# Kernel optimization log

Hardware: AMD Instinct MI355X
Metric: run time of the kernel (lower is better)

Reference implementation:

```python
import jax, jax.numpy as jnp
import numpy as np

D = 1024

def setup_inputs() -> dict:
    key = jax.random.key(0)
    ks = jax.random.split(key, 9)
    s = 1.0 / np.sqrt(D)
    return {
        "x": jax.random.normal(ks[0], (4, 2048, D), dtype=jnp.float32),
        "y": jax.random.normal(ks[1], (4, 2048, D), dtype=jnp.float32),
        "z": jax.random.normal(ks[2], (4, 2048, D), dtype=jnp.float32),
        "Wq": jax.random.uniform(ks[3], (D, D), jnp.float32, -s, s),
        "bq": jax.random.uniform(ks[4], (D,), jnp.float32, -s, s),
        "Wk": jax.random.uniform(ks[5], (D, D), jnp.float32, -s, s),
        "bk": jax.random.uniform(ks[6], (D,), jnp.float32, -s, s),
        "Wv": jax.random.uniform(ks[7], (D, D), jnp.float32, -s, s),
        "bv": jax.random.uniform(ks[8], (D,), jnp.float32, -s, s),
    }

def reference(x, y, z, Wq, bq, Wk, bk, Wv, bv):
    # nn.Linear: x @ W^T + b
    Q = jnp.einsum('bsd,ed->bse', x, Wq) + bq  # [B,S,D]
    K = jnp.einsum('bsd,ed->bse', y, Wk) + bk
    V = jnp.einsum('bsd,ed->bse', z, Wv) + bv
    scores = jnp.einsum('bqd,bkd->bqk', Q, K) / jnp.sqrt(jnp.float32(Q.shape[-1]))
    weights = jax.nn.softmax(scores, axis=-1)  # [B,S,S]
    return jnp.einsum('bqk,bkd->bqd', weights, V)
```

## Files before the change

kernel.cpp:

```cpp
#include <hip/hip_runtime.h>
#include <hip/hip_bf16.h>

typedef unsigned short u16;
typedef __bf16 bf16x8 __attribute__((ext_vector_type(8)));
typedef float  f32x4  __attribute__((ext_vector_type(4)));
typedef u16    u16x8  __attribute__((ext_vector_type(8)));

__device__ __forceinline__ u16 f2bf(float f) {
    unsigned u = __float_as_uint(f);
    u = (u + 0x7fffu + ((u >> 16) & 1u)) >> 16;
    return (u16)u;
}
__device__ __forceinline__ float bf2f(u16 h) {
    return __uint_as_float(((unsigned)h) << 16);
}

__global__ __launch_bounds__(256) void cvt3_bf16_kernel(
    const float* __restrict__ s0, const float* __restrict__ s1,
    const float* __restrict__ s2, u16* __restrict__ dst, size_t dstride, int n8)
{
    int i = blockIdx.x * 256 + threadIdx.x;
    if (i >= n8) return;
    const float* src = (blockIdx.z == 0) ? s0 : (blockIdx.z == 1) ? s1 : s2;
    u16* d = dst + (size_t)blockIdx.z * dstride;
    const float4* s4 = (const float4*)src;
    float4 a = s4[2 * i], b = s4[2 * i + 1];
    u16x8 o;
    o[0] = f2bf(a.x); o[1] = f2bf(a.y); o[2] = f2bf(a.z); o[3] = f2bf(a.w);
    o[4] = f2bf(b.x); o[5] = f2bf(b.y); o[6] = f2bf(b.z); o[7] = f2bf(b.w);
    ((u16x8*)d)[i] = o;
}

#define BUF_U 12288
#define LDS_B (3 * BUF_U * 2)

__device__ __forceinline__ void gload_lds16(const void* g, void* l) {
    __builtin_amdgcn_global_load_lds(
        (__attribute__((address_space(1))) void*)g,
        (__attribute__((address_space(3))) void*)l, 16, 0, 0);
}

__device__ __forceinline__ int swz_g(int r) {
    return (r & 3) ^ (((r >> 2) & 1) << 1) ^ ((r >> 3) & 1);
}

template<bool OUT_BF16, bool HAS_BIAS>
__global__ __launch_bounds__(512, 4) void gemm_k32(
    const u16* __restrict__ A, const u16* __restrict__ Bm,
    const float* __restrict__ bias, void* __restrict__ C,
    int M, int N, int K, float scale,
    long long aBS, long long bBS, long long cBS)
{
    extern __shared__ u16 lds[];

    const int gx = gridDim.x, gy = gridDim.y;
    const int slab = gx * gy;
    const int nwg  = slab * gridDim.z;
    const int b    = blockIdx.x + gx * (blockIdx.y + gy * blockIdx.z);
    const int qc   = nwg >> 3;
    const int L    = (b & 7) * qc + (b >> 3);
    const int tz   = L / slab;
    const int rr   = L - tz * slab;
    const int g4   = rr / (gx * 4);
    const int w4   = rr - g4 * (gx * 4);
    const int tx   = w4 >> 2;
    const int ty   = g4 * 4 + (w4 & 3);

    A  += (size_t)tz * aBS;
    Bm += (size_t)tz * bBS;

    const int m0 = ty * 256;
    const int n0 = tx * 128;
    const int tid  = threadIdx.x;
    const int lane = tid & 63;
    const int wave = tid >> 6;
    const int wm   = wave >> 1;
    const int wn   = wave & 1;
    const int fr   = lane & 15;
    const int kg   = lane >> 4;

    const int r_ = tid >> 2;
    const int s_ = (tid & 3) ^ swz_g(r_);
    const u16* gA = A  + (size_t)(m0 + r_) * K + s_ * 8;
    const u16* gB = Bm + (size_t)(n0 + r_) * K + s_ * 8;
    const int dstW = wave * 512;

    auto stA = [&](u16* bufb, int tk, int c) {
        gload_lds16(gA + (size_t)c * 128 * K + tk * 32, bufb + c * 4096 + dstW);
    };
    auto stB = [&](u16* bufb, int tk) {
        gload_lds16(gB + tk * 32, bufb + 8192 + dstW);
    };

    auto rdA = [&](const u16* sa, int m) {
        const int R  = wm * 64 + m * 16 + fr;
        const int sl = kg ^ swz_g(R);
        return *(const bf16x8*)&sa[R * 32 + sl * 8];
    };
    auto rdB = [&](const u16* sb, int n) {
        const int R  = wn * 64 + n * 16 + fr;
        const int sl = kg ^ swz_g(R);
        return *(const bf16x8*)&sb[R * 32 + sl * 8];
    };

    f32x4 acc[4][4] = {};
    const int NT = K / 32;

    u16 *p0 = lds, *p1 = lds + BUF_U, *p2 = lds + 2 * BUF_U;

    stA(p0, 0, 0); stA(p0, 0, 1); stB(p0, 0);
    stA(p1, 1, 0); stA(p1, 1, 1); stB(p1, 1);
    asm volatile("s_waitcnt vmcnt(3)" ::: "memory");
    __builtin_amdgcn_s_barrier();

    for (int t = 0; t < NT; ++t) {
        const bool st = (t + 2 < NT);
        if (st) { stA(p2, t + 2, 0); stA(p2, t + 2, 1); stB(p2, t + 2); }

        bf16x8 a[4], bfr[4];
        #pragma unroll
        for (int m = 0; m < 4; ++m) a[m] = rdA(p0, m);
        #pragma unroll
        for (int n = 0; n < 4; ++n) bfr[n] = rdB(p0 + 8192, n);

        __builtin_amdgcn_s_setprio(1);
        #pragma unroll
        for (int m = 0; m < 4; ++m)
            #pragma unroll
            for (int n = 0; n < 4; ++n)
                acc[m][n] = __builtin_amdgcn_mfma_f32_16x16x32_bf16(
                    a[m], bfr[n], acc[m][n], 0, 0, 0);
        __builtin_amdgcn_s_setprio(0);

        if (t + 1 < NT) {
            if (st) asm volatile("s_waitcnt vmcnt(3)" ::: "memory");
            else    asm volatile("s_waitcnt vmcnt(0)" ::: "memory");
            __builtin_amdgcn_s_barrier();
        }
        u16* tmp = p0; p0 = p1; p1 = p2; p2 = tmp;
    }

    if (OUT_BF16) {
        u16* Cb = (u16*)C + (size_t)tz * cBS;
        #pragma unroll
        for (int m = 0; m < 4; ++m) {
            const int row0 = m0 + wm * 64 + m * 16 + kg * 4;
            #pragma unroll
            for (int n = 0; n < 4; ++n) {
                const int col = n0 + wn * 64 + n * 16 + fr;
                const float badd = HAS_BIAS ? bias[col] : 0.0f;
                f32x4 v = acc[m][n];
                #pragma unroll
                for (int q = 0; q < 4; ++q)
                    Cb[(size_t)(row0 + q) * N + col] = f2bf(v[q] * scale + badd);
            }
        }
    } else {
        float* Cf = (float*)C + (size_t)tz * cBS;
        #pragma unroll
        for (int m = 0; m < 4; ++m) {
            const int row0 = m0 + wm * 64 + m * 16 + kg * 4;
            #pragma unroll
            for (int n = 0; n < 4; ++n) {
                const int col = n0 + wn * 64 + n * 16 + fr;
                const float badd = HAS_BIAS ? bias[col] : 0.0f;
                f32x4 v = acc[m][n];
                #pragma unroll
                for (int q = 0; q < 4; ++q)
                    Cf[(size_t)(row0 + q) * N + col] = v[q] * scale + badd;
            }
        }
    }
}

__global__ __launch_bounds__(256) void transpose_bf16(
    const u16* __restrict__ V, u16* __restrict__ Vt)
{
    __shared__ u16 tile[64][72];
    const int b  = blockIdx.z;
    const int k0 = blockIdx.y * 64;
    const int d0 = blockIdx.x * 64;
    const int tr = threadIdx.x >> 3;
    const int tc = (threadIdx.x & 7) * 8;

    const u16* src = V + ((size_t)b * 2048 + k0) * 1024 + d0;
    #pragma unroll
    for (int i = 0; i < 2; ++i) {
        int r = tr + i * 32;
        *(u16x8*)&tile[r][tc] = *(const u16x8*)&src[(size_t)r * 1024 + tc];
    }
    __syncthreads();
    u16* dst = Vt + ((size_t)b * 1024 + d0) * 2048 + k0;
    #pragma unroll
    for (int i = 0; i < 2; ++i) {
        int r = tr + i * 32;
        u16x8 o;
        #pragma unroll
        for (int j = 0; j < 8; ++j) o[j] = tile[tc + j][r];
        *(u16x8*)&dst[(size_t)r * 2048 + tc] = o;
    }
}

__global__ __launch_bounds__(256) void softmax_kernel(u16* __restrict__ SP)
{
    const size_t row = blockIdx.x;
    u16x8* rp = (u16x8*)(SP + row * 2048);
    const int tid  = threadIdx.x;
    const int lane = tid & 63;
    const int wv   = tid >> 6;

    u16x8 v = rp[tid];
    float f[8];
    #pragma unroll
    for (int j = 0; j < 8; ++j) f[j] = bf2f(v[j]);

    float m = f[0];
    #pragma unroll
    for (int j = 1; j < 8; ++j) m = fmaxf(m, f[j]);
    #pragma unroll
    for (int o = 32; o; o >>= 1) m = fmaxf(m, __shfl_xor(m, o, 64));

    __shared__ float red[8];
    if (lane == 0) red[wv] = m;
    __syncthreads();
    m = fmaxf(fmaxf(red[0], red[1]), fmaxf(red[2], red[3]));

    float e[8], s = 0.f;
    #pragma unroll
    for (int j = 0; j < 8; ++j) { e[j] = __expf(f[j] - m); s += e[j]; }
    #pragma unroll
    for (int o = 32; o; o >>= 1) s += __shfl_xor(s, o, 64);
    if (lane == 0) red[4 + wv] = s;
    __syncthreads();
    s = (red[4] + red[5]) + (red[6] + red[7]);
    const float inv = 1.0f / s;

    u16x8 o8;
    #pragma unroll
    for (int j = 0; j < 8; ++j) o8[j] = f2bf(e[j] * inv);
    rp[tid] = o8;
}

extern "C" void kernel_launch(void* const* d_in, const int* in_sizes, int n_in,
                              void* d_out, int out_size, void* d_ws, size_t ws_size,
                              hipStream_t stream)
{
    const int Bn = 4, S = 2048, D = 1024;
    const size_t nx = (size_t)Bn * S * D;
    const size_t nw = (size_t)D * D;

    const float* x  = (const float*)d_in[0];
    const float* y  = (const float*)d_in[1];
    const float* z  = (const float*)d_in[2];
    const float* Wq = (const float*)d_in[3];
    const float* bq = (const float*)d_in[4];
    const float* Wk = (const float*)d_in[5];
    const float* bk = (const float*)d_in[6];
    const float* Wv = (const float*)d_in[7];
    const float* bv = (const float*)d_in[8];

    u16* xb  = (u16*)d_ws;
    u16* yb  = xb + nx;
    u16* zb  = yb + nx;
    u16* wqb = zb + nx;
    u16* wkb = wqb + nw;
    u16* wvb = wkb + nw;
    u16* Qb  = wvb + nw;
    u16* Kb  = Qb + nx;
    u16* Vb  = Kb + nx;
    u16* Vt  = Vb + nx;
    u16* Pb  = xb;

    hipFuncSetAttribute((const void*)gemm_k32<true,  true >,
                        hipFuncAttributeMaxDynamicSharedMemorySize, LDS_B);
    hipFuncSetAttribute((const void*)gemm_k32<true,  false>,
                        hipFuncAttributeMaxDynamicSharedMemorySize, LDS_B);
    hipFuncSetAttribute((const void*)gemm_k32<false, false>,
                        hipFuncAttributeMaxDynamicSharedMemorySize, LDS_B);

    const int n8x = (int)(nx / 8), n8w = (int)(nw / 8);
    cvt3_bf16_kernel<<<dim3((n8x + 255) / 256, 1, 3), 256, 0, stream>>>(
        x, y, z, xb, nx, n8x);
    cvt3_bf16_kernel<<<dim3((n8w + 255) / 256, 1, 3), 256, 0, stream>>>(
        Wq, Wk, Wv, wqb, nw, n8w);

    dim3 gQKV(D / 128, (Bn * S) / 256, 1);
    gemm_k32<true, true><<<gQKV, 512, LDS_B, stream>>>(xb, wqb, bq, Qb, Bn * S, D, D, 1.0f, 0, 0, 0);
    gemm_k32<true, true><<<gQKV, 512, LDS_B, stream>>>(yb, wkb, bk, Kb, Bn * S, D, D, 1.0f, 0, 0, 0);
    gemm_k32<true, true><<<gQKV, 512, LDS_B, stream>>>(zb, wvb, bv, Vb, Bn * S, D, D, 1.0f, 0, 0, 0);

    transpose_bf16<<<dim3(D / 64, S / 64, Bn), 256, 0, stream>>>(Vb, Vt);

    gemm_k32<true, false><<<dim3(S / 128, S / 256, Bn), 512, LDS_B, stream>>>(
        Qb, Kb, nullptr, Pb, S, S, D, 0.03125f,
        (long long)S * D, (long long)S * D, (long long)S * S);

    softmax_kernel<<<Bn * S, 256, 0, stream>>>(Pb);

    gemm_k32<false, false><<<dim3(D / 128, S / 256, Bn), 512, LDS_B, stream>>>(
        Pb, Vt, nullptr, d_out, S, D, S, 1.0f,
        (long long)S * S, (long long)D * S, (long long)S * D);
}
```

Baseline: 332.0 us.

## Rewrite GEMM with BK=64 double buffering and larger per-wave tiles

Replaces the K=32 triple-buffered GEMM with a K=64 double-buffered kernel. The waves now form a 2x4 grid, each owning a 128-row strip, and the tile width is a template parameter, set to 256 for the scores GEMM and 128 elsewhere. The goal is more MFMA work per LDS load and per barrier and more operand reuse, at the cost of more accumulator registers and a lower occupancy bound (2 blocks per CU instead of 4). Extra barriers inside each K step guard the fragment reads, and the LDS swizzle becomes an XOR on 8-element chunks.

```diff
diff --git a/kernel.cpp b/kernel.cpp
--- a/kernel.cpp
+++ b/kernel.cpp
@@ -31,26 +31,23 @@
     ((u16x8*)d)[i] = o;
 }
 
-#define BUF_U 12288
-#define LDS_B (3 * BUF_U * 2)
-
 __device__ __forceinline__ void gload_lds16(const void* g, void* l) {
     __builtin_amdgcn_global_load_lds(
         (__attribute__((address_space(1))) void*)g,
         (__attribute__((address_space(3))) void*)l, 16, 0, 0);
 }
 
-__device__ __forceinline__ int swz_g(int r) {
-    return (r & 3) ^ (((r >> 2) & 1) << 1) ^ ((r >> 3) & 1);
-}
-
-template<bool OUT_BF16, bool HAS_BIAS>
-__global__ __launch_bounds__(512, 4) void gemm_k32(
+template<int BN_, bool OUT_BF16, bool HAS_BIAS>
+__global__ __launch_bounds__(512, 2) void gemm_c8(
     const u16* __restrict__ A, const u16* __restrict__ Bm,
     const float* __restrict__ bias, void* __restrict__ C,
     int M, int N, int K, float scale,
     long long aBS, long long bBS, long long cBS)
 {
+    constexpr int NF   = BN_ / 64;
+    constexpr int NB   = (BN_ * 64 * 2) / 8192;
+    constexpr int BUFU = 16384 + BN_ * 64;
+    constexpr int WN   = BN_ / 4;
     extern __shared__ u16 lds[];
 
     const int gx = gridDim.x, gy = gridDim.y;
@@ -70,86 +67,103 @@
     Bm += (size_t)tz * bBS;
 
     const int m0 = ty * 256;
-    const int n0 = tx * 128;
+    const int n0 = tx * BN_;
     const int tid  = threadIdx.x;
     const int lane = tid & 63;
     const int wave = tid >> 6;
-    const int wm   = wave >> 1;
-    const int wn   = wave & 1;
+    const int wm   = wave >> 2;
+    const int wn   = wave & 3;
     const int fr   = lane & 15;
     const int kg   = lane >> 4;
 
-    const int r_ = tid >> 2;
-    const int s_ = (tid & 3) ^ swz_g(r_);
-    const u16* gA = A  + (size_t)(m0 + r_) * K + s_ * 8;
-    const u16* gB = Bm + (size_t)(n0 + r_) * K + s_ * 8;
+    const int r_  = tid >> 3;
+    const int sw8 = ((tid & 7) ^ (r_ & 7)) * 8;
+    const u16* gA = A  + (size_t)(m0 + r_) * K + sw8;
+    const u16* gB = Bm + (size_t)(n0 + r_) * K + sw8;
     const int dstW = wave * 512;
 
-    auto stA = [&](u16* bufb, int tk, int c) {
-        gload_lds16(gA + (size_t)c * 128 * K + tk * 32, bufb + c * 4096 + dstW);
+    auto stage = [&](int db, int t) {
+        u16* dst = lds + db * BUFU;
+        #pragma unroll
+        for (int c = 0; c < 4; ++c)
+            gload_lds16(gA + (size_t)c * 64 * K + t * 64, dst + c * 4096 + dstW);
+        #pragma unroll
+        for (int c = 0; c < NB; ++c)
+            gload_lds16(gB + (size_t)c * 64 * K + t * 64, dst + 16384 + c * 4096 + dstW);
     };
-    auto stB = [&](u16* bufb, int tk) {
-        gload_lds16(gB + tk * 32, bufb + 8192 + dstW);
+
+    auto rdT = [&](const u16* base, int R, int ck) {
+        return *(const bf16x8*)&base[R * 64 + ((ck ^ (R & 7)) << 3)];
     };
 
-    auto rdA = [&](const u16* sa, int m) {
-        const int R  = wm * 64 + m * 16 + fr;
-        const int sl = kg ^ swz_g(R);
-        return *(const bf16x8*)&sa[R * 32 + sl * 8];
-    };
-    auto rdB = [&](const u16* sb, int n) {
-        const int R  = wn * 64 + n * 16 + fr;
-        const int sl = kg ^ swz_g(R);
-        return *(const bf16x8*)&sb[R * 32 + sl * 8];
-    };
-
-    f32x4 acc[4][4] = {};
-    const int NT = K / 32;
-
-    u16 *p0 = lds, *p1 = lds + BUF_U, *p2 = lds + 2 * BUF_U;
-
-    stA(p0, 0, 0); stA(p0, 0, 1); stB(p0, 0);
-    stA(p1, 1, 0); stA(p1, 1, 1); stB(p1, 1);
-    asm volatile("s_waitcnt vmcnt(3)" ::: "memory");
-    __builtin_amdgcn_s_barrier();
-
-    for (int t = 0; t < NT; ++t) {
-        const bool st = (t + 2 < NT);
-        if (st) { stA(p2, t + 2, 0); stA(p2, t + 2, 1); stB(p2, t + 2); }
-
-        bf16x8 a[4], bfr[4];
-        #pragma unroll
-        for (int m = 0; m < 4; ++m) a[m] = rdA(p0, m);
-        #pragma unroll
-        for (int n = 0; n < 4; ++n) bfr[n] = rdB(p0 + 8192, n);
-
-        __builtin_amdgcn_s_setprio(1);
-        #pragma unroll
-        for (int m = 0; m < 4; ++m)
+    f32x4 acc[8][NF] = {};
+    bf16x8 bF[NF][2];
+    const int NT = K / 64;
+
+    stage(0, 0);
+    stage(1, 1);
+    if constexpr (NB == 4) asm volatile("s_waitcnt vmcnt(8)" ::: "memory");
+    else                   asm volatile("s_waitcnt vmcnt(6)" ::: "memory");
+    asm volatile("s_barrier" ::: "memory");
+
+    for (int i = 0; i < NT / 2; ++i) {
+        const int t = 2 * i;
+        #pragma unroll
+        for (int half = 0; half < 2; ++half) {
+            const u16* sa = lds + half * BUFU;
+            const u16* sb = sa + 16384;
+
             #pragma unroll
-            for (int n = 0; n < 4; ++n)
-                acc[m][n] = __builtin_amdgcn_mfma_f32_16x16x32_bf16(
-                    a[m], bfr[n], acc[m][n], 0, 0, 0);
-        __builtin_amdgcn_s_setprio(0);
-
-        if (t + 1 < NT) {
-            if (st) asm volatile("s_waitcnt vmcnt(3)" ::: "memory");
-            else    asm volatile("s_waitcnt vmcnt(0)" ::: "memory");
-            __builtin_amdgcn_s_barrier();
+            for (int q = 0; q < 4; ++q) {
+                if (q == 0) {
+                    #pragma unroll
+                    for (int nf = 0; nf < NF; ++nf)
+                        #pragma unroll
+                        for (int ks = 0; ks < 2; ++ks)
+                            bF[nf][ks] = rdT(sb, wn * WN + nf * 16 + fr, ks * 4 + kg);
+                }
+                bf16x8 aF[2][2];
+                #pragma unroll
+                for (int mi = 0; mi < 2; ++mi)
+                    #pragma unroll
+                    for (int ks = 0; ks < 2; ++ks)
+                        aF[mi][ks] = rdT(sa, wm * 128 + q * 32 + mi * 16 + fr, ks * 4 + kg);
+
+                __builtin_amdgcn_s_setprio(1);
+                #pragma unroll
+                for (int mi = 0; mi < 2; ++mi)
+                    #pragma unroll
+                    for (int nf = 0; nf < NF; ++nf)
+                        #pragma unroll
+                        for (int ks = 0; ks < 2; ++ks)
+                            acc[q * 2 + mi][nf] = __builtin_amdgcn_mfma_f32_16x16x32_bf16(
+                                aF[mi][ks], bF[nf][ks], acc[q * 2 + mi][nf], 0, 0, 0);
+                __builtin_amdgcn_s_setprio(0);
+                asm volatile("s_barrier" ::: "memory");
+            }
+
+            const int tn = t + half + 2;
+            if (tn < NT) {
+                stage(half, tn);
+                if constexpr (NB == 4) asm volatile("s_waitcnt vmcnt(8)" ::: "memory");
+                else                   asm volatile("s_waitcnt vmcnt(6)" ::: "memory");
+            } else {
+                asm volatile("s_waitcnt vmcnt(0)" ::: "memory");
+            }
+            asm volatile("s_barrier" ::: "memory");
         }
-        u16* tmp = p0; p0 = p1; p1 = p2; p2 = tmp;
     }
 
     if (OUT_BF16) {
         u16* Cb = (u16*)C + (size_t)tz * cBS;
         #pragma unroll
-        for (int m = 0; m < 4; ++m) {
-            const int row0 = m0 + wm * 64 + m * 16 + kg * 4;
+        for (int mf = 0; mf < 8; ++mf) {
+            const int row0 = m0 + wm * 128 + mf * 16 + kg * 4;
             #pragma unroll
-            for (int n = 0; n < 4; ++n) {
-                const int col = n0 + wn * 64 + n * 16 + fr;
+            for (int nf = 0; nf < NF; ++nf) {
+                const int col = n0 + wn * WN + nf * 16 + fr;
                 const float badd = HAS_BIAS ? bias[col] : 0.0f;
-                f32x4 v = acc[m][n];
+                f32x4 v = acc[mf][nf];
                 #pragma unroll
                 for (int q = 0; q < 4; ++q)
                     Cb[(size_t)(row0 + q) * N + col] = f2bf(v[q] * scale + badd);
@@ -158,13 +172,13 @@
     } else {
         float* Cf = (float*)C + (size_t)tz * cBS;
         #pragma unroll
-        for (int m = 0; m < 4; ++m) {
-            const int row0 = m0 + wm * 64 + m * 16 + kg * 4;
+        for (int mf = 0; mf < 8; ++mf) {
+            const int row0 = m0 + wm * 128 + mf * 16 + kg * 4;
             #pragma unroll
-            for (int n = 0; n < 4; ++n) {
-                const int col = n0 + wn * 64 + n * 16 + fr;
+            for (int nf = 0; nf < NF; ++nf) {
+                const int col = n0 + wn * WN + nf * 16 + fr;
                 const float badd = HAS_BIAS ? bias[col] : 0.0f;
-                f32x4 v = acc[m][n];
+                f32x4 v = acc[mf][nf];
                 #pragma unroll
                 for (int q = 0; q < 4; ++q)
                     Cf[(size_t)(row0 + q) * N + col] = v[q] * scale + badd;
@@ -271,12 +285,15 @@
     u16* Vt  = Vb + nx;
     u16* Pb  = xb;
 
-    hipFuncSetAttribute((const void*)gemm_k32<true,  true >,
-                        hipFuncAttributeMaxDynamicSharedMemorySize, LDS_B);
-    hipFuncSetAttribute((const void*)gemm_k32<true,  false>,
-                        hipFuncAttributeMaxDynamicSharedMemorySize, LDS_B);
-    hipFuncSetAttribute((const void*)gemm_k32<false, false>,
-                        hipFuncAttributeMaxDynamicSharedMemorySize, LDS_B);
+    const int LDS_QKV = (16384 + 128 * 64) * 2 * 2;
+    const int LDS_SC  = (16384 + 256 * 64) * 2 * 2;
+
+    hipFuncSetAttribute((const void*)gemm_c8<128, true,  true >,
+                        hipFuncAttributeMaxDynamicSharedMemorySize, LDS_QKV);
+    hipFuncSetAttribute((const void*)gemm_c8<256, true,  false>,
+                        hipFuncAttributeMaxDynamicSharedMemorySize, LDS_SC);
+    hipFuncSetAttribute((const void*)gemm_c8<128, false, false>,
+                        hipFuncAttributeMaxDynamicSharedMemorySize, LDS_QKV);
 
     const int n8x = (int)(nx / 8), n8w = (int)(nw / 8);
     cvt3_bf16_kernel<<<dim3((n8x + 255) / 256, 1, 3), 256, 0, stream>>>(
@@ -285,19 +302,22 @@
         Wq, Wk, Wv, wqb, nw, n8w);
 
     dim3 gQKV(D / 128, (Bn * S) / 256, 1);
-    gemm_k32<true, true><<<gQKV, 512, LDS_B, stream>>>(xb, wqb, bq, Qb, Bn * S, D, D, 1.0f, 0, 0, 0);
-    gemm_k32<true, true><<<gQKV, 512, LDS_B, stream>>>(yb, wkb, bk, Kb, Bn * S, D, D, 1.0f, 0, 0, 0);
-    gemm_k32<true, true><<<gQKV, 512, LDS_B, stream>>>(zb, wvb, bv, Vb, Bn * S, D, D, 1.0f, 0, 0, 0);
+    gemm_c8<128, true, true><<<gQKV, 512, LDS_QKV, stream>>>(
+        xb, wqb, bq, Qb, Bn * S, D, D, 1.0f, 0, 0, 0);
+    gemm_c8<128, true, true><<<gQKV, 512, LDS_QKV, stream>>>(
+        yb, wkb, bk, Kb, Bn * S, D, D, 1.0f, 0, 0, 0);
+    gemm_c8<128, true, true><<<gQKV, 512, LDS_QKV, stream>>>(
+        zb, wvb, bv, Vb, Bn * S, D, D, 1.0f, 0, 0, 0);
 
     transpose_bf16<<<dim3(D / 64, S / 64, Bn), 256, 0, stream>>>(Vb, Vt);
 
-    gemm_k32<true, false><<<dim3(S / 128, S / 256, Bn), 512, LDS_B, stream>>>(
+    gemm_c8<256, true, false><<<dim3(S / 256, S / 256, Bn), 512, LDS_SC, stream>>>(
         Qb, Kb, nullptr, Pb, S, S, D, 0.03125f,
         (long long)S * D, (long long)S * D, (long long)S * S);
 
     softmax_kernel<<<Bn * S, 256, 0, stream>>>(Pb);
 
-    gemm_k32<false, false><<<dim3(D / 128, S / 256, Bn), 512, LDS_B, stream>>>(
+    gemm_c8<128, false, false><<<dim3(D / 128, S / 256, Bn), 512, LDS_QKV, stream>>>(
         Pb, Vt, nullptr, d_out, S, D, S, 1.0f,
         (long long)S * S, (long long)D * S, (long long)S * D);
 }
```

Measured after the change: 323.2 us. 1.03x faster.
